# Performance work log

Hardware: AMD Instinct MI355X
Metric: run time of the kernel (lower is better)

The kernel has to match this reference:

```python
import jax, jax.numpy as jnp
import numpy as np

B, T, H, OUT = 128, 1024, 256, 2


def setup_inputs() -> dict:
    key = jax.random.key(0)
    ks = jax.random.split(key, 16)
    s_in = 1.0 / np.sqrt(1 + H)
    s_2h = 1.0 / np.sqrt(2 * H)
    s_o = 1.0 / np.sqrt(H)
    return {
        "x": jax.random.normal(ks[0], (B, T, 2), dtype=jnp.float32),
        "h_0": jax.random.normal(ks[1], (1, B, H), dtype=jnp.float32) * 0.1,
        "Wa": jax.random.normal(ks[2], (1 + H, H), dtype=jnp.float32) * s_in,
        "ba": jnp.zeros((H,), dtype=jnp.float32),
        "Wp1": jax.random.normal(ks[3], (1 + H, H), dtype=jnp.float32) * s_in,
        "bp1": jnp.zeros((H,), dtype=jnp.float32),
        "Wp2": jax.random.normal(ks[4], (1 + H, H), dtype=jnp.float32) * s_in,
        "bp2": jnp.zeros((H,), dtype=jnp.float32),
        "Wz": jax.random.normal(ks[5], (2 * H, H), dtype=jnp.float32) * s_2h,
        "bz": jnp.zeros((H,), dtype=jnp.float32),
        "Wh": jax.random.normal(ks[6], (2 * H, H), dtype=jnp.float32) * s_2h,
        "bh": jnp.zeros((H,), dtype=jnp.float32),
        "Wo": jax.random.normal(ks[7], (H, OUT), dtype=jnp.float32) * s_o,
        "bo": jnp.zeros((OUT,), dtype=jnp.float32),
    }


def _pgjanet_scan(x, h0, Wa, ba, Wp1, bp1, Wp2, bp2, Wz, bz, Wh, bh):
    # x: [B, T, 2], h0: [B, H]
    xt_all = jnp.swapaxes(x, 0, 1)  # [T, B, 2]

    def step(h, xt):
        amp = xt[:, 0:1]                       # [B, 1]
        ph = xt[:, 1:2]                        # [B, 1]
        a = jnp.tanh(jnp.concatenate([amp, h], axis=-1) @ Wa + ba)
        p1 = jnp.tanh(jnp.concatenate([jnp.cos(ph), h], axis=-1) @ Wp1 + bp1)
        p2 = jnp.tanh(jnp.concatenate([jnp.sin(ph), h], axis=-1) @ Wp2 + bp2)
        u = a * p1 * p2 * (1 - a) * (1 - p1) * (1 - p2)
        newin = jnp.concatenate([u, h], axis=-1)  # [B, 2H]
        z = jax.nn.sigmoid(newin @ Wz + bz)
        h_cand = jnp.tanh(newin @ Wh + bh)
        h_new = z * h + (1 - z) * h_cand
        return h_new, h_new

    h_n, hs = jax.lax.scan(step, h0, xt_all)
    return jnp.swapaxes(hs, 0, 1), h_n  # [B, T, H], [B, H]


def reference(x, h_0, Wa, ba, Wp1, bp1, Wp2, bp2, Wz, bz, Wh, bh, Wo, bo):
    hs, h_n = _pgjanet_scan(x, h_0[0], Wa, ba, Wp1, bp1, Wp2, bp2, Wz, bz, Wh, bh)
    out = hs @ Wo + bo  # [B, T, OUT]
    return (out, h_n)
```

## Files before the change

### kernel.cpp

```cpp
#include <hip/hip_runtime.h>
#include <math.h>


#define B_   128
#define T_   1024
#define H_   256
#define GB   16
#define GC   16
#define MB   8
#define NS   16
#define NTHR 512
#define HPAD 264

typedef float    f32x4 __attribute__((ext_vector_type(4)));
typedef unsigned u32x4 __attribute__((ext_vector_type(4)));

__device__ __forceinline__ void sys_st_x4(unsigned* p, u32x4 v) {
  asm volatile("global_store_dwordx4 %0, %1, off sc0 sc1" :: "v"(p), "v"(v) : "memory");
}
__device__ __forceinline__ void sys_ld2_x4(const unsigned* p0, const unsigned* p1,
                                           u32x4& a, u32x4& b) {
  asm volatile("global_load_dwordx4 %0, %2, off sc0 sc1\n\t"
               "global_load_dwordx4 %1, %3, off sc0 sc1\n\t"
               "s_waitcnt vmcnt(0)"
               : "=&v"(a), "=&v"(b) : "v"(p0), "v"(p1) : "memory");
}

__launch_bounds__(NTHR, 1)
__global__ void pgjanet_persist(
    const float* __restrict__ x,   const float* __restrict__ h0,
    const float* __restrict__ Wa,  const float* __restrict__ ba,
    const float* __restrict__ Wp1, const float* __restrict__ bp1,
    const float* __restrict__ Wp2, const float* __restrict__ bp2,
    const float* __restrict__ Wz,  const float* __restrict__ bz,
    const float* __restrict__ Wh,  const float* __restrict__ bh,
    const float* __restrict__ Wo,  const float* __restrict__ bo,
    float* __restrict__ out,
    unsigned* __restrict__ u_ex,
    unsigned* __restrict__ h_ex)
{
  __shared__ __align__(16) float w1t[3 * NS * 256];
  __shared__ __align__(16) float w2t[2 * NS * 512];
  __shared__ __align__(16) float h_lds[MB * HPAD];
  __shared__ __align__(16) float u_lds[MB * HPAD];
  __shared__ __align__(16) float wo_s[H_ * 2];
  __shared__ __align__(16) float xin[2 * MB * 4];

  const int wg   = blockIdx.x;
  const int g    = wg >> 4;
  const int gc   = wg & (GC - 1);
  const int tid  = threadIdx.x;
  const int lane = tid & 63;
  const int wave = tid >> 6;
  const int mb   = lane >> 3;
  const int ks   = lane & 7;
  const int b0   = g * MB;
  const int n0   = gc * NS + wave * 2;

  for (int i = tid; i < 3 * NS * 256; i += NTHR) {
    int c = i >> 8, k = i & 255;
    int mat = c >> 4, n = c & 15;
    const float* W = (mat == 0) ? Wa : (mat == 1 ? Wp1 : Wp2);
    w1t[i] = W[(1 + k) * H_ + gc * NS + n];
  }
  for (int i = tid; i < 2 * NS * 512; i += NTHR) {
    int c = i >> 9, k = i & 511;
    int mat = c >> 4, n = c & 15;
    const float* W = (mat == 0) ? Wz : Wh;
    w2t[i] = W[k * H_ + gc * NS + n];
  }
  for (int i = tid; i < H_ * 2; i += NTHR) wo_s[i] = Wo[i];

  float w1r0_[6], b1_[6];
#pragma unroll
  for (int m = 0; m < 3; ++m) {
    const float* W  = (m == 0) ? Wa : (m == 1 ? Wp1 : Wp2);
    const float* bb = (m == 0) ? ba : (m == 1 ? bp1 : bp2);
#pragma unroll
    for (int cc = 0; cc < 2; ++cc) {
      w1r0_[m * 2 + cc] = W[n0 + cc];
      b1_[m * 2 + cc]   = bb[n0 + cc];
    }
  }
  float bz_[2] = { bz[n0], bz[n0 + 1] };
  float bh_[2] = { bh[n0], bh[n0 + 1] };
  const float bo0 = bo[0], bo1 = bo[1];

  {
    int flat = tid * 4;
    int mbb = flat >> 8, kk = flat & 255;
    *(f32x4*)(h_lds + mbb * HPAD + kk) = *(const f32x4*)(h0 + (b0 + mbb) * H_ + kk);
  }
  if (tid < MB) {
    float2 xt = *(const float2*)(x + ((b0 + tid) * T_) * 2);
    f32x4 xi; xi[0] = xt.x; xi[1] = cosf(xt.y); xi[2] = sinf(xt.y); xi[3] = 0.f;
    *(f32x4*)(xin + tid * 4) = xi;
  }
  __syncthreads();

  unsigned* u_exg = u_ex + g * 4096;
  unsigned* h_exg = h_ex + g * 4096;
  unsigned* u_my  = u_exg + ((gc * 8 + wave) * 8) * 4;
  unsigned* h_my  = h_exg + ((gc * 8 + wave) * 8) * 4;

  for (int t = 0; t < T_; ++t) {
    const unsigned seq = (unsigned)(t + 1);

    f32x4 hv[8];
#pragma unroll
    for (int kt = 0; kt < 8; ++kt)
      hv[kt] = *(const f32x4*)(h_lds + mb * HPAD + kt * 32 + ks * 4);

    float acc[6] = {0.f, 0.f, 0.f, 0.f, 0.f, 0.f};
#pragma unroll
    for (int kt = 0; kt < 8; ++kt) {
      f32x4 h4 = hv[kt];
#pragma unroll
      for (int m = 0; m < 3; ++m)
#pragma unroll
        for (int cc = 0; cc < 2; ++cc) {
          f32x4 w4 = *(const f32x4*)(w1t + (m * NS + wave * 2 + cc) * 256 + kt * 32 + ks * 4);
          float s = acc[m * 2 + cc];
          s = fmaf(h4[0], w4[0], s); s = fmaf(h4[1], w4[1], s);
          s = fmaf(h4[2], w4[2], s); s = fmaf(h4[3], w4[3], s);
          acc[m * 2 + cc] = s;
        }
    }
#pragma unroll
    for (int i = 0; i < 6; ++i) {
      float v = acc[i];
      v += __shfl_xor(v, 1);
      v += __shfl_xor(v, 2);
      v += __shfl_xor(v, 4);
      acc[i] = v;
    }
    if (ks == 0) {
      f32x4 xi = *(const f32x4*)(xin + ((t & 1) * MB + mb) * 4);
      float uu[2];
#pragma unroll
      for (int cc = 0; cc < 2; ++cc) {
        float a  = tanhf(acc[0 + cc] + xi[0] * w1r0_[0 + cc] + b1_[0 + cc]);
        float p1 = tanhf(acc[2 + cc] + xi[1] * w1r0_[2 + cc] + b1_[2 + cc]);
        float p2 = tanhf(acc[4 + cc] + xi[2] * w1r0_[4 + cc] + b1_[4 + cc]);
        uu[cc] = a * p1 * p2 * (1.f - a) * (1.f - p1) * (1.f - p2);
      }
      u32x4 ch;
      ch.x = __float_as_uint(uu[0]); ch.y = __float_as_uint(uu[1]);
      ch.z = seq; ch.w = 0u;
      sys_st_x4(u_my + mb * 4, ch);
    }

    if (t + 1 < T_ && tid < MB) {
      float2 xt = *(const float2*)(x + ((b0 + tid) * T_ + (t + 1)) * 2);
      f32x4 xi; xi[0] = xt.x; xi[1] = cosf(xt.y); xi[2] = sinf(xt.y); xi[3] = 0.f;
      *(f32x4*)(xin + (((t + 1) & 1) * MB + tid) * 4) = xi;
    }
    if (t > 0 && ((t - 1) & 15) == gc) {
      f32x4 h4  = *(const f32x4*)(h_lds + wave * HPAD + lane * 4);
      f32x4 wo0 = *(const f32x4*)(wo_s + lane * 8);
      f32x4 wo1 = *(const f32x4*)(wo_s + lane * 8 + 4);
      float v0 = h4[0] * wo0[0] + h4[1] * wo0[2] + h4[2] * wo1[0] + h4[3] * wo1[2];
      float v1 = h4[0] * wo0[1] + h4[1] * wo0[3] + h4[2] * wo1[1] + h4[3] * wo1[3];
      v0 += __shfl_xor(v0, 1);  v1 += __shfl_xor(v1, 1);
      v0 += __shfl_xor(v0, 2);  v1 += __shfl_xor(v1, 2);
      v0 += __shfl_xor(v0, 4);  v1 += __shfl_xor(v1, 4);
      v0 += __shfl_xor(v0, 8);  v1 += __shfl_xor(v1, 8);
      v0 += __shfl_xor(v0, 16); v1 += __shfl_xor(v1, 16);
      v0 += __shfl_xor(v0, 32); v1 += __shfl_xor(v1, 32);
      if (lane == 0) {
        float2 o; o.x = v0 + bo0; o.y = v1 + bo1;
        *(float2*)(out + ((b0 + wave) * T_ + (t - 1)) * 2) = o;
      }
    }
    float acc2[4] = {0.f, 0.f, 0.f, 0.f};
#pragma unroll
    for (int kt = 0; kt < 8; ++kt) {
      f32x4 h4 = hv[kt];
#pragma unroll
      for (int m = 0; m < 2; ++m)
#pragma unroll
        for (int cc = 0; cc < 2; ++cc) {
          f32x4 w4 = *(const f32x4*)(w2t + (m * NS + wave * 2 + cc) * 512 + 256 + kt * 32 + ks * 4);
          float s = acc2[m * 2 + cc];
          s = fmaf(h4[0], w4[0], s); s = fmaf(h4[1], w4[1], s);
          s = fmaf(h4[2], w4[2], s); s = fmaf(h4[3], w4[3], s);
          acc2[m * 2 + cc] = s;
        }
    }

    {
      u32x4 A, B;
      const unsigned* p0 = u_exg + tid * 4;
      const unsigned* p1 = u_exg + (tid + 512) * 4;
      for (;;) {
        sys_ld2_x4(p0, p1, A, B);
        if (A.z == seq && B.z == seq) break;
        __builtin_amdgcn_s_sleep(1);
      }
      int c = tid;
      float2 d0; d0.x = __uint_as_float(A.x); d0.y = __uint_as_float(A.y);
      *(float2*)(u_lds + (c & 7) * HPAD + (c >> 6) * 16 + ((c >> 3) & 7) * 2) = d0;
      c = tid + 512;
      float2 d1; d1.x = __uint_as_float(B.x); d1.y = __uint_as_float(B.y);
      *(float2*)(u_lds + (c & 7) * HPAD + (c >> 6) * 16 + ((c >> 3) & 7) * 2) = d1;
    }
    __syncthreads();

#pragma unroll
    for (int kt = 0; kt < 8; ++kt) {
      f32x4 u4 = *(const f32x4*)(u_lds + mb * HPAD + kt * 32 + ks * 4);
#pragma unroll
      for (int m = 0; m < 2; ++m)
#pragma unroll
        for (int cc = 0; cc < 2; ++cc) {
          f32x4 w4 = *(const f32x4*)(w2t + (m * NS + wave * 2 + cc) * 512 + kt * 32 + ks * 4);
          float s = acc2[m * 2 + cc];
          s = fmaf(u4[0], w4[0], s); s = fmaf(u4[1], w4[1], s);
          s = fmaf(u4[2], w4[2], s); s = fmaf(u4[3], w4[3], s);
          acc2[m * 2 + cc] = s;
        }
    }
#pragma unroll
    for (int i = 0; i < 4; ++i) {
      float v = acc2[i];
      v += __shfl_xor(v, 1);
      v += __shfl_xor(v, 2);
      v += __shfl_xor(v, 4);
      acc2[i] = v;
    }
    if (ks == 0) {
      float z0  = 1.f / (1.f + expf(-(acc2[0] + bz_[0])));
      float z1  = 1.f / (1.f + expf(-(acc2[1] + bz_[1])));
      float hc0 = tanhf(acc2[2] + bh_[0]);
      float hc1 = tanhf(acc2[3] + bh_[1]);
      float2 hp = *(const float2*)(h_lds + mb * HPAD + n0);
      float hn0 = z0 * hp.x + (1.f - z0) * hc0;
      float hn1 = z1 * hp.y + (1.f - z1) * hc1;
      u32x4 ch;
      ch.x = __float_as_uint(hn0); ch.y = __float_as_uint(hn1);
      ch.z = seq; ch.w = 0u;
      sys_st_x4(h_my + mb * 4, ch);
      if (t == T_ - 1) {
        float2 o; o.x = hn0; o.y = hn1;
        *(float2*)(out + B_ * T_ * 2 + (b0 + mb) * H_ + n0) = o;
      }
    }
    __syncthreads();

    {
      u32x4 A, B;
      const unsigned* p0 = h_exg + tid * 4;
      const unsigned* p1 = h_exg + (tid + 512) * 4;
      for (;;) {
        sys_ld2_x4(p0, p1, A, B);
        if (A.z == seq && B.z == seq) break;
        __builtin_amdgcn_s_sleep(1);
      }
      int c = tid;
      float2 d0; d0.x = __uint_as_float(A.x); d0.y = __uint_as_float(A.y);
      *(float2*)(h_lds + (c & 7) * HPAD + (c >> 6) * 16 + ((c >> 3) & 7) * 2) = d0;
      c = tid + 512;
      float2 d1; d1.x = __uint_as_float(B.x); d1.y = __uint_as_float(B.y);
      *(float2*)(h_lds + (c & 7) * HPAD + (c >> 6) * 16 + ((c >> 3) & 7) * 2) = d1;
    }
    __syncthreads();
  }

  if (gc == ((T_ - 1) & 15)) {
    f32x4 h4  = *(const f32x4*)(h_lds + wave * HPAD + lane * 4);
    f32x4 wo0 = *(const f32x4*)(wo_s + lane * 8);
    f32x4 wo1 = *(const f32x4*)(wo_s + lane * 8 + 4);
    float v0 = h4[0] * wo0[0] + h4[1] * wo0[2] + h4[2] * wo1[0] + h4[3] * wo1[2];
    float v1 = h4[0] * wo0[1] + h4[1] * wo0[3] + h4[2] * wo1[1] + h4[3] * wo1[3];
    v0 += __shfl_xor(v0, 1);  v1 += __shfl_xor(v1, 1);
    v0 += __shfl_xor(v0, 2);  v1 += __shfl_xor(v1, 2);
    v0 += __shfl_xor(v0, 4);  v1 += __shfl_xor(v1, 4);
    v0 += __shfl_xor(v0, 8);  v1 += __shfl_xor(v1, 8);
    v0 += __shfl_xor(v0, 16); v1 += __shfl_xor(v1, 16);
    v0 += __shfl_xor(v0, 32); v1 += __shfl_xor(v1, 32);
    if (lane == 0) {
      float2 o; o.x = v0 + bo0; o.y = v1 + bo1;
      *(float2*)(out + ((b0 + wave) * T_ + (T_ - 1)) * 2) = o;
    }
  }
}

extern "C" void kernel_launch(void* const* d_in, const int* in_sizes, int n_in,
                              void* d_out, int out_size, void* d_ws, size_t ws_size,
                              hipStream_t stream) {
  (void)in_sizes; (void)n_in; (void)out_size; (void)ws_size;
  const float* x   = (const float*)d_in[0];
  const float* h0  = (const float*)d_in[1];
  const float* Wa  = (const float*)d_in[2];
  const float* ba  = (const float*)d_in[3];
  const float* Wp1 = (const float*)d_in[4];
  const float* bp1 = (const float*)d_in[5];
  const float* Wp2 = (const float*)d_in[6];
  const float* bp2 = (const float*)d_in[7];
  const float* Wz  = (const float*)d_in[8];
  const float* bz  = (const float*)d_in[9];
  const float* Wh  = (const float*)d_in[10];
  const float* bh  = (const float*)d_in[11];
  const float* Wo  = (const float*)d_in[12];
  const float* bo  = (const float*)d_in[13];

  float* out = (float*)d_out;
  char*  ws  = (char*)d_ws;
  unsigned* u_ex = (unsigned*)ws;
  unsigned* h_ex = (unsigned*)(ws + 262144);

  hipMemsetAsync(ws, 0, 524288, stream);

  pgjanet_persist<<<dim3(GB * GC), dim3(NTHR), 0, stream>>>(
      x, h0, Wa, ba, Wp1, bp1, Wp2, bp2, Wz, bz, Wh, bh, Wo, bo,
      out, u_ex, h_ex);
}
```

Baseline: 5.698 ms.

## Split batch into two halves per wave, widen K-split, use fast tanh/sigmoid

Each wave now handles two groups of four batch rows with a 16-way K split instead of eight rows with an 8-way split. Each weight vector loaded from LDS is reused for both halves in the h-part of the second GEMV. The exchange layout is reordered so each thread polls two adjacent 16-byte slots from one base pointer, and the first half's u is published earlier. tanhf/expf are replaced by clamped __expf with a hardware reciprocal, which is cheaper but slightly less accurate.

```diff
diff --git a/kernel.cpp b/kernel.cpp
--- a/kernel.cpp
+++ b/kernel.cpp
@@ -18,12 +18,21 @@
 __device__ __forceinline__ void sys_st_x4(unsigned* p, u32x4 v) {
   asm volatile("global_store_dwordx4 %0, %1, off sc0 sc1" :: "v"(p), "v"(v) : "memory");
 }
-__device__ __forceinline__ void sys_ld2_x4(const unsigned* p0, const unsigned* p1,
-                                           u32x4& a, u32x4& b) {
+__device__ __forceinline__ void sys_ld_pair(const unsigned* p, u32x4& a, u32x4& b) {
   asm volatile("global_load_dwordx4 %0, %2, off sc0 sc1\n\t"
-               "global_load_dwordx4 %1, %3, off sc0 sc1\n\t"
+               "global_load_dwordx4 %1, %2, off offset:16 sc0 sc1\n\t"
                "s_waitcnt vmcnt(0)"
-               : "=&v"(a), "=&v"(b) : "v"(p0), "v"(p1) : "memory");
+               : "=&v"(a), "=&v"(b) : "v"(p) : "memory");
+}
+
+__device__ __forceinline__ float ftanh(float x) {
+  x = fminf(fmaxf(x, -15.f), 15.f);
+  float e = __expf(-2.f * x);
+  return (1.f - e) * __builtin_amdgcn_rcpf(1.f + e);
+}
+__device__ __forceinline__ float fsigm(float x) {
+  x = fminf(fmaxf(x, -30.f), 30.f);
+  return __builtin_amdgcn_rcpf(1.f + __expf(-x));
 }
 
 __launch_bounds__(NTHR, 1)
@@ -52,8 +61,8 @@
   const int tid  = threadIdx.x;
   const int lane = tid & 63;
   const int wave = tid >> 6;
-  const int mb   = lane >> 3;
-  const int ks   = lane & 7;
+  const int mbl  = lane >> 4;
+  const int ks   = lane & 15;
   const int b0   = g * MB;
   const int n0   = gc * NS + wave * 2;
 
@@ -87,8 +96,7 @@
   const float bo0 = bo[0], bo1 = bo[1];
 
   {
-    int flat = tid * 4;
-    int mbb = flat >> 8, kk = flat & 255;
+    int mbb = tid >> 6, kk = (tid & 63) * 4;
     *(f32x4*)(h_lds + mbb * HPAD + kk) = *(const f32x4*)(h0 + (b0 + mbb) * H_ + kk);
   }
   if (tid < MB) {
@@ -100,54 +108,101 @@
 
   unsigned* u_exg = u_ex + g * 4096;
   unsigned* h_exg = h_ex + g * 4096;
-  unsigned* u_my  = u_exg + ((gc * 8 + wave) * 8) * 4;
-  unsigned* h_my  = h_exg + ((gc * 8 + wave) * 8) * 4;
+  unsigned* u_my = u_exg + (((gc * 8 + wave) * 4 + mbl) * 2) * 4;
+  unsigned* h_my = h_exg + (((gc * 8 + wave) * 4 + mbl) * 2) * 4;
+  const unsigned* pu = u_exg + tid * 8;
+  const unsigned* ph = h_exg + tid * 8;
+  const int ccol = (tid >> 5) * 16 + ((tid >> 2) & 7) * 2;
+  const int cmb  = tid & 3;
 
   for (int t = 0; t < T_; ++t) {
     const unsigned seq = (unsigned)(t + 1);
 
-    f32x4 hv[8];
-#pragma unroll
-    for (int kt = 0; kt < 8; ++kt)
-      hv[kt] = *(const f32x4*)(h_lds + mb * HPAD + kt * 32 + ks * 4);
-
-    float acc[6] = {0.f, 0.f, 0.f, 0.f, 0.f, 0.f};
-#pragma unroll
-    for (int kt = 0; kt < 8; ++kt) {
-      f32x4 h4 = hv[kt];
-#pragma unroll
-      for (int m = 0; m < 3; ++m)
-#pragma unroll
-        for (int cc = 0; cc < 2; ++cc) {
-          f32x4 w4 = *(const f32x4*)(w1t + (m * NS + wave * 2 + cc) * 256 + kt * 32 + ks * 4);
-          float s = acc[m * 2 + cc];
-          s = fmaf(h4[0], w4[0], s); s = fmaf(h4[1], w4[1], s);
-          s = fmaf(h4[2], w4[2], s); s = fmaf(h4[3], w4[3], s);
-          acc[m * 2 + cc] = s;
-        }
-    }
-#pragma unroll
-    for (int i = 0; i < 6; ++i) {
-      float v = acc[i];
-      v += __shfl_xor(v, 1);
-      v += __shfl_xor(v, 2);
-      v += __shfl_xor(v, 4);
-      acc[i] = v;
-    }
-    if (ks == 0) {
-      f32x4 xi = *(const f32x4*)(xin + ((t & 1) * MB + mb) * 4);
-      float uu[2];
-#pragma unroll
-      for (int cc = 0; cc < 2; ++cc) {
-        float a  = tanhf(acc[0 + cc] + xi[0] * w1r0_[0 + cc] + b1_[0 + cc]);
-        float p1 = tanhf(acc[2 + cc] + xi[1] * w1r0_[2 + cc] + b1_[2 + cc]);
-        float p2 = tanhf(acc[4 + cc] + xi[2] * w1r0_[4 + cc] + b1_[4 + cc]);
-        uu[cc] = a * p1 * p2 * (1.f - a) * (1.f - p1) * (1.f - p2);
-      }
-      u32x4 ch;
-      ch.x = __float_as_uint(uu[0]); ch.y = __float_as_uint(uu[1]);
-      ch.z = seq; ch.w = 0u;
-      sys_st_x4(u_my + mb * 4, ch);
+    f32x4 hvA[4], hvB[4];
+    float acc2A[4] = {0.f, 0.f, 0.f, 0.f};
+    float acc2B[4] = {0.f, 0.f, 0.f, 0.f};
+
+#pragma unroll
+    for (int kt = 0; kt < 4; ++kt)
+      hvA[kt] = *(const f32x4*)(h_lds + mbl * HPAD + kt * 64 + ks * 4);
+    {
+      float acc[6] = {0.f, 0.f, 0.f, 0.f, 0.f, 0.f};
+#pragma unroll
+      for (int kt = 0; kt < 4; ++kt) {
+        f32x4 h4 = hvA[kt];
+#pragma unroll
+        for (int m = 0; m < 3; ++m)
+#pragma unroll
+          for (int cc = 0; cc < 2; ++cc) {
+            f32x4 w4 = *(const f32x4*)(w1t + (m * NS + wave * 2 + cc) * 256 + kt * 64 + ks * 4);
+            float s = acc[m * 2 + cc];
+            s = fmaf(h4[0], w4[0], s); s = fmaf(h4[1], w4[1], s);
+            s = fmaf(h4[2], w4[2], s); s = fmaf(h4[3], w4[3], s);
+            acc[m * 2 + cc] = s;
+          }
+      }
+#pragma unroll
+      for (int i = 0; i < 6; ++i) {
+        float v = acc[i];
+        v += __shfl_xor(v, 1); v += __shfl_xor(v, 2);
+        v += __shfl_xor(v, 4); v += __shfl_xor(v, 8);
+        acc[i] = v;
+      }
+      if (ks == 0) {
+        f32x4 xi = *(const f32x4*)(xin + ((t & 1) * MB + mbl) * 4);
+        float a0  = ftanh(acc[0] + xi[0] * w1r0_[0] + b1_[0]);
+        float a1  = ftanh(acc[1] + xi[0] * w1r0_[1] + b1_[1]);
+        float p10 = ftanh(acc[2] + xi[1] * w1r0_[2] + b1_[2]);
+        float p11 = ftanh(acc[3] + xi[1] * w1r0_[3] + b1_[3]);
+        float p20 = ftanh(acc[4] + xi[2] * w1r0_[4] + b1_[4]);
+        float p21 = ftanh(acc[5] + xi[2] * w1r0_[5] + b1_[5]);
+        u32x4 ch;
+        ch.x = __float_as_uint(a0 * p10 * p20 * (1.f - a0) * (1.f - p10) * (1.f - p20));
+        ch.y = __float_as_uint(a1 * p11 * p21 * (1.f - a1) * (1.f - p11) * (1.f - p21));
+        ch.z = seq; ch.w = 0u;
+        sys_st_x4(u_my, ch);
+      }
+    }
+#pragma unroll
+    for (int kt = 0; kt < 4; ++kt)
+      hvB[kt] = *(const f32x4*)(h_lds + (4 + mbl) * HPAD + kt * 64 + ks * 4);
+    {
+      float acc[6] = {0.f, 0.f, 0.f, 0.f, 0.f, 0.f};
+#pragma unroll
+      for (int kt = 0; kt < 4; ++kt) {
+        f32x4 h4 = hvB[kt];
+#pragma unroll
+        for (int m = 0; m < 3; ++m)
+#pragma unroll
+          for (int cc = 0; cc < 2; ++cc) {
+            f32x4 w4 = *(const f32x4*)(w1t + (m * NS + wave * 2 + cc) * 256 + kt * 64 + ks * 4);
+            float s = acc[m * 2 + cc];
+            s = fmaf(h4[0], w4[0], s); s = fmaf(h4[1], w4[1], s);
+            s = fmaf(h4[2], w4[2], s); s = fmaf(h4[3], w4[3], s);
+            acc[m * 2 + cc] = s;
+          }
+      }
+#pragma unroll
+      for (int i = 0; i < 6; ++i) {
+        float v = acc[i];
+        v += __shfl_xor(v, 1); v += __shfl_xor(v, 2);
+        v += __shfl_xor(v, 4); v += __shfl_xor(v, 8);
+        acc[i] = v;
+      }
+      if (ks == 0) {
+        f32x4 xi = *(const f32x4*)(xin + ((t & 1) * MB + 4 + mbl) * 4);
+        float a0  = ftanh(acc[0] + xi[0] * w1r0_[0] + b1_[0]);
+        float a1  = ftanh(acc[1] + xi[0] * w1r0_[1] + b1_[1]);
+        float p10 = ftanh(acc[2] + xi[1] * w1r0_[2] + b1_[2]);
+        float p11 = ftanh(acc[3] + xi[1] * w1r0_[3] + b1_[3]);
+        float p20 = ftanh(acc[4] + xi[2] * w1r0_[4] + b1_[4]);
+        float p21 = ftanh(acc[5] + xi[2] * w1r0_[5] + b1_[5]);
+        u32x4 ch;
+        ch.x = __float_as_uint(a0 * p10 * p20 * (1.f - a0) * (1.f - p10) * (1.f - p20));
+        ch.y = __float_as_uint(a1 * p11 * p21 * (1.f - a1) * (1.f - p11) * (1.f - p21));
+        ch.z = seq; ch.w = 0u;
+        sys_st_x4(u_my + 4, ch);
+      }
     }
 
     if (t + 1 < T_ && tid < MB) {
@@ -172,96 +227,126 @@
         *(float2*)(out + ((b0 + wave) * T_ + (t - 1)) * 2) = o;
       }
     }
-    float acc2[4] = {0.f, 0.f, 0.f, 0.f};
-#pragma unroll
-    for (int kt = 0; kt < 8; ++kt) {
-      f32x4 h4 = hv[kt];
+#pragma unroll
+    for (int kt = 0; kt < 4; ++kt) {
+      f32x4 hA = hvA[kt], hB = hvB[kt];
 #pragma unroll
       for (int m = 0; m < 2; ++m)
 #pragma unroll
         for (int cc = 0; cc < 2; ++cc) {
-          f32x4 w4 = *(const f32x4*)(w2t + (m * NS + wave * 2 + cc) * 512 + 256 + kt * 32 + ks * 4);
-          float s = acc2[m * 2 + cc];
-          s = fmaf(h4[0], w4[0], s); s = fmaf(h4[1], w4[1], s);
-          s = fmaf(h4[2], w4[2], s); s = fmaf(h4[3], w4[3], s);
-          acc2[m * 2 + cc] = s;
+          f32x4 w4 = *(const f32x4*)(w2t + (m * NS + wave * 2 + cc) * 512 + 256 + kt * 64 + ks * 4);
+          float sa = acc2A[m * 2 + cc], sb = acc2B[m * 2 + cc];
+          sa = fmaf(hA[0], w4[0], sa); sa = fmaf(hA[1], w4[1], sa);
+          sa = fmaf(hA[2], w4[2], sa); sa = fmaf(hA[3], w4[3], sa);
+          sb = fmaf(hB[0], w4[0], sb); sb = fmaf(hB[1], w4[1], sb);
+          sb = fmaf(hB[2], w4[2], sb); sb = fmaf(hB[3], w4[3], sb);
+          acc2A[m * 2 + cc] = sa; acc2B[m * 2 + cc] = sb;
         }
     }
 
     {
-      u32x4 A, B;
-      const unsigned* p0 = u_exg + tid * 4;
-      const unsigned* p1 = u_exg + (tid + 512) * 4;
+      u32x4 A, Bc;
       for (;;) {
-        sys_ld2_x4(p0, p1, A, B);
-        if (A.z == seq && B.z == seq) break;
+        sys_ld_pair(pu, A, Bc);
+        if (A.z == seq && Bc.z == seq) break;
         __builtin_amdgcn_s_sleep(1);
       }
-      int c = tid;
-      float2 d0; d0.x = __uint_as_float(A.x); d0.y = __uint_as_float(A.y);
-      *(float2*)(u_lds + (c & 7) * HPAD + (c >> 6) * 16 + ((c >> 3) & 7) * 2) = d0;
-      c = tid + 512;
-      float2 d1; d1.x = __uint_as_float(B.x); d1.y = __uint_as_float(B.y);
-      *(float2*)(u_lds + (c & 7) * HPAD + (c >> 6) * 16 + ((c >> 3) & 7) * 2) = d1;
+      float2 d0; d0.x = __uint_as_float(A.x);  d0.y = __uint_as_float(A.y);
+      float2 d1; d1.x = __uint_as_float(Bc.x); d1.y = __uint_as_float(Bc.y);
+      *(float2*)(u_lds + cmb * HPAD + ccol)       = d0;
+      *(float2*)(u_lds + (cmb + 4) * HPAD + ccol) = d1;
     }
     __syncthreads();
 
 #pragma unroll
-    for (int kt = 0; kt < 8; ++kt) {
-      f32x4 u4 = *(const f32x4*)(u_lds + mb * HPAD + kt * 32 + ks * 4);
+    for (int kt = 0; kt < 4; ++kt) {
+      f32x4 u4 = *(const f32x4*)(u_lds + mbl * HPAD + kt * 64 + ks * 4);
 #pragma unroll
       for (int m = 0; m < 2; ++m)
 #pragma unroll
         for (int cc = 0; cc < 2; ++cc) {
-          f32x4 w4 = *(const f32x4*)(w2t + (m * NS + wave * 2 + cc) * 512 + kt * 32 + ks * 4);
-          float s = acc2[m * 2 + cc];
+          f32x4 w4 = *(const f32x4*)(w2t + (m * NS + wave * 2 + cc) * 512 + kt * 64 + ks * 4);
+          float s = acc2A[m * 2 + cc];
           s = fmaf(u4[0], w4[0], s); s = fmaf(u4[1], w4[1], s);
           s = fmaf(u4[2], w4[2], s); s = fmaf(u4[3], w4[3], s);
-          acc2[m * 2 + cc] = s;
+          acc2A[m * 2 + cc] = s;
         }
     }
 #pragma unroll
     for (int i = 0; i < 4; ++i) {
-      float v = acc2[i];
-      v += __shfl_xor(v, 1);
-      v += __shfl_xor(v, 2);
-      v += __shfl_xor(v, 4);
-      acc2[i] = v;
+      float v = acc2A[i];
+      v += __shfl_xor(v, 1); v += __shfl_xor(v, 2);
+      v += __shfl_xor(v, 4); v += __shfl_xor(v, 8);
+      acc2A[i] = v;
     }
     if (ks == 0) {
-      float z0  = 1.f / (1.f + expf(-(acc2[0] + bz_[0])));
-      float z1  = 1.f / (1.f + expf(-(acc2[1] + bz_[1])));
-      float hc0 = tanhf(acc2[2] + bh_[0]);
-      float hc1 = tanhf(acc2[3] + bh_[1]);
-      float2 hp = *(const float2*)(h_lds + mb * HPAD + n0);
+      float z0  = fsigm(acc2A[0] + bz_[0]);
+      float z1  = fsigm(acc2A[1] + bz_[1]);
+      float hc0 = ftanh(acc2A[2] + bh_[0]);
+      float hc1 = ftanh(acc2A[3] + bh_[1]);
+      float2 hp = *(const float2*)(h_lds + mbl * HPAD + n0);
       float hn0 = z0 * hp.x + (1.f - z0) * hc0;
       float hn1 = z1 * hp.y + (1.f - z1) * hc1;
       u32x4 ch;
       ch.x = __float_as_uint(hn0); ch.y = __float_as_uint(hn1);
       ch.z = seq; ch.w = 0u;
-      sys_st_x4(h_my + mb * 4, ch);
+      sys_st_x4(h_my, ch);
       if (t == T_ - 1) {
         float2 o; o.x = hn0; o.y = hn1;
-        *(float2*)(out + B_ * T_ * 2 + (b0 + mb) * H_ + n0) = o;
+        *(float2*)(out + B_ * T_ * 2 + (b0 + mbl) * H_ + n0) = o;
+      }
+    }
+#pragma unroll
+    for (int kt = 0; kt < 4; ++kt) {
+      f32x4 u4 = *(const f32x4*)(u_lds + (4 + mbl) * HPAD + kt * 64 + ks * 4);
+#pragma unroll
+      for (int m = 0; m < 2; ++m)
+#pragma unroll
+        for (int cc = 0; cc < 2; ++cc) {
+          f32x4 w4 = *(const f32x4*)(w2t + (m * NS + wave * 2 + cc) * 512 + kt * 64 + ks * 4);
+          float s = acc2B[m * 2 + cc];
+          s = fmaf(u4[0], w4[0], s); s = fmaf(u4[1], w4[1], s);
+          s = fmaf(u4[2], w4[2], s); s = fmaf(u4[3], w4[3], s);
+          acc2B[m * 2 + cc] = s;
+        }
+    }
+#pragma unroll
+    for (int i = 0; i < 4; ++i) {
+      float v = acc2B[i];
+      v += __shfl_xor(v, 1); v += __shfl_xor(v, 2);
+      v += __shfl_xor(v, 4); v += __shfl_xor(v, 8);
+      acc2B[i] = v;
+    }
+    if (ks == 0) {
+      float z0  = fsigm(acc2B[0] + bz_[0]);
+      float z1  = fsigm(acc2B[1] + bz_[1]);
+      float hc0 = ftanh(acc2B[2] + bh_[0]);
+      float hc1 = ftanh(acc2B[3] + bh_[1]);
+      float2 hp = *(const float2*)(h_lds + (4 + mbl) * HPAD + n0);
+      float hn0 = z0 * hp.x + (1.f - z0) * hc0;
+      float hn1 = z1 * hp.y + (1.f - z1) * hc1;
+      u32x4 ch;
+      ch.x = __float_as_uint(hn0); ch.y = __float_as_uint(hn1);
+      ch.z = seq; ch.w = 0u;
+      sys_st_x4(h_my + 4, ch);
+      if (t == T_ - 1) {
+        float2 o; o.x = hn0; o.y = hn1;
+        *(float2*)(out + B_ * T_ * 2 + (b0 + 4 + mbl) * H_ + n0) = o;
       }
     }
     __syncthreads();
 
     {
-      u32x4 A, B;
-      const unsigned* p0 = h_exg + tid * 4;
-      const unsigned* p1 = h_exg + (tid + 512) * 4;
+      u32x4 A, Bc;
       for (;;) {
-        sys_ld2_x4(p0, p1, A, B);
-        if (A.z == seq && B.z == seq) break;
+        sys_ld_pair(ph, A, Bc);
+        if (A.z == seq && Bc.z == seq) break;
         __builtin_amdgcn_s_sleep(1);
       }
-      int c = tid;
-      float2 d0; d0.x = __uint_as_float(A.x); d0.y = __uint_as_float(A.y);
-      *(float2*)(h_lds + (c & 7) * HPAD + (c >> 6) * 16 + ((c >> 3) & 7) * 2) = d0;
-      c = tid + 512;
-      float2 d1; d1.x = __uint_as_float(B.x); d1.y = __uint_as_float(B.y);
-      *(float2*)(h_lds + (c & 7) * HPAD + (c >> 6) * 16 + ((c >> 3) & 7) * 2) = d1;
+      float2 d0; d0.x = __uint_as_float(A.x);  d0.y = __uint_as_float(A.y);
+      float2 d1; d1.x = __uint_as_float(Bc.x); d1.y = __uint_as_float(Bc.y);
+      *(float2*)(h_lds + cmb * HPAD + ccol)       = d0;
+      *(float2*)(h_lds + (cmb + 4) * HPAD + ccol) = d1;
     }
     __syncthreads();
   }
```

Result: slower. 6.873 ms (+20.6%).

## Split hidden columns across 32 smaller workgroups and use fast tanh/sigmoid

Applied to the files above, without the earlier changes.

Doubles the number of workgroups per batch group (each now owns 8 hidden columns with 256 threads), so per-step matmul work per workgroup halves and two workgroups can share a CU. The exchange polling is reorganised so each thread loads four contiguous 16-byte chunks with one base pointer. Library tanhf/expf are replaced by clamped exp plus hardware reciprocal approximations. The trade-off is more workgroups taking part in each per-step global flag exchange, which may raise synchronisation latency, and slightly lower accuracy in the activations.

```diff
diff --git a/kernel.cpp b/kernel.cpp
--- a/kernel.cpp
+++ b/kernel.cpp
@@ -6,10 +6,10 @@
 #define T_   1024
 #define H_   256
 #define GB   16
-#define GC   16
+#define GC   32
 #define MB   8
-#define NS   16
-#define NTHR 512
+#define NS   8
+#define NTHR 256
 #define HPAD 264
 
 typedef float    f32x4 __attribute__((ext_vector_type(4)));
@@ -18,15 +18,27 @@
 __device__ __forceinline__ void sys_st_x4(unsigned* p, u32x4 v) {
   asm volatile("global_store_dwordx4 %0, %1, off sc0 sc1" :: "v"(p), "v"(v) : "memory");
 }
-__device__ __forceinline__ void sys_ld2_x4(const unsigned* p0, const unsigned* p1,
-                                           u32x4& a, u32x4& b) {
-  asm volatile("global_load_dwordx4 %0, %2, off sc0 sc1\n\t"
-               "global_load_dwordx4 %1, %3, off sc0 sc1\n\t"
+__device__ __forceinline__ void sys_ld_quad(const unsigned* p, u32x4& a, u32x4& b,
+                                            u32x4& c, u32x4& d) {
+  asm volatile("global_load_dwordx4 %0, %4, off sc0 sc1\n\t"
+               "global_load_dwordx4 %1, %4, off offset:16 sc0 sc1\n\t"
+               "global_load_dwordx4 %2, %4, off offset:32 sc0 sc1\n\t"
+               "global_load_dwordx4 %3, %4, off offset:48 sc0 sc1\n\t"
                "s_waitcnt vmcnt(0)"
-               : "=&v"(a), "=&v"(b) : "v"(p0), "v"(p1) : "memory");
-}
-
-__launch_bounds__(NTHR, 1)
+               : "=&v"(a), "=&v"(b), "=&v"(c), "=&v"(d) : "v"(p) : "memory");
+}
+
+__device__ __forceinline__ float ftanh(float x) {
+  x = fminf(fmaxf(x, -15.f), 15.f);
+  float e = __expf(-2.f * x);
+  return (1.f - e) * __builtin_amdgcn_rcpf(1.f + e);
+}
+__device__ __forceinline__ float fsigm(float x) {
+  x = fminf(fmaxf(x, -30.f), 30.f);
+  return __builtin_amdgcn_rcpf(1.f + __expf(-x));
+}
+
+__launch_bounds__(NTHR, 2)
 __global__ void pgjanet_persist(
     const float* __restrict__ x,   const float* __restrict__ h0,
     const float* __restrict__ Wa,  const float* __restrict__ ba,
@@ -47,7 +59,7 @@
   __shared__ __align__(16) float xin[2 * MB * 4];
 
   const int wg   = blockIdx.x;
-  const int g    = wg >> 4;
+  const int g    = wg >> 5;
   const int gc   = wg & (GC - 1);
   const int tid  = threadIdx.x;
   const int lane = tid & 63;
@@ -59,13 +71,13 @@
 
   for (int i = tid; i < 3 * NS * 256; i += NTHR) {
     int c = i >> 8, k = i & 255;
-    int mat = c >> 4, n = c & 15;
+    int mat = c >> 3, n = c & 7;
     const float* W = (mat == 0) ? Wa : (mat == 1 ? Wp1 : Wp2);
     w1t[i] = W[(1 + k) * H_ + gc * NS + n];
   }
   for (int i = tid; i < 2 * NS * 512; i += NTHR) {
     int c = i >> 9, k = i & 511;
-    int mat = c >> 4, n = c & 15;
+    int mat = c >> 3, n = c & 7;
     const float* W = (mat == 0) ? Wz : Wh;
     w2t[i] = W[k * H_ + gc * NS + n];
   }
@@ -87,9 +99,9 @@
   const float bo0 = bo[0], bo1 = bo[1];
 
   {
-    int flat = tid * 4;
-    int mbb = flat >> 8, kk = flat & 255;
-    *(f32x4*)(h_lds + mbb * HPAD + kk) = *(const f32x4*)(h0 + (b0 + mbb) * H_ + kk);
+    int mbb = tid >> 5, kk = (tid & 31) * 8;
+    *(f32x4*)(h_lds + mbb * HPAD + kk)     = *(const f32x4*)(h0 + (b0 + mbb) * H_ + kk);
+    *(f32x4*)(h_lds + mbb * HPAD + kk + 4) = *(const f32x4*)(h0 + (b0 + mbb) * H_ + kk + 4);
   }
   if (tid < MB) {
     float2 xt = *(const float2*)(x + ((b0 + tid) * T_) * 2);
@@ -100,8 +112,12 @@
 
   unsigned* u_exg = u_ex + g * 4096;
   unsigned* h_exg = h_ex + g * 4096;
-  unsigned* u_my  = u_exg + ((gc * 8 + wave) * 8) * 4;
-  unsigned* h_my  = h_exg + ((gc * 8 + wave) * 8) * 4;
+  unsigned* u_my  = u_exg + ((gc * 4 + wave) * 8) * 4;
+  unsigned* h_my  = h_exg + ((gc * 4 + wave) * 8) * 4;
+  const unsigned* pu = u_exg + tid * 16;
+  const unsigned* ph = h_exg + tid * 16;
+  const int crow0 = (tid & 1) * 4;
+  const int ccol  = (tid >> 1) * 2;
 
   for (int t = 0; t < T_; ++t) {
     const unsigned seq = (unsigned)(t + 1);
@@ -129,23 +145,20 @@
 #pragma unroll
     for (int i = 0; i < 6; ++i) {
       float v = acc[i];
-      v += __shfl_xor(v, 1);
-      v += __shfl_xor(v, 2);
-      v += __shfl_xor(v, 4);
+      v += __shfl_xor(v, 1); v += __shfl_xor(v, 2); v += __shfl_xor(v, 4);
       acc[i] = v;
     }
     if (ks == 0) {
       f32x4 xi = *(const f32x4*)(xin + ((t & 1) * MB + mb) * 4);
-      float uu[2];
-#pragma unroll
-      for (int cc = 0; cc < 2; ++cc) {
-        float a  = tanhf(acc[0 + cc] + xi[0] * w1r0_[0 + cc] + b1_[0 + cc]);
-        float p1 = tanhf(acc[2 + cc] + xi[1] * w1r0_[2 + cc] + b1_[2 + cc]);
-        float p2 = tanhf(acc[4 + cc] + xi[2] * w1r0_[4 + cc] + b1_[4 + cc]);
-        uu[cc] = a * p1 * p2 * (1.f - a) * (1.f - p1) * (1.f - p2);
-      }
+      float a0  = ftanh(acc[0] + xi[0] * w1r0_[0] + b1_[0]);
+      float a1  = ftanh(acc[1] + xi[0] * w1r0_[1] + b1_[1]);
+      float p10 = ftanh(acc[2] + xi[1] * w1r0_[2] + b1_[2]);
+      float p11 = ftanh(acc[3] + xi[1] * w1r0_[3] + b1_[3]);
+      float p20 = ftanh(acc[4] + xi[2] * w1r0_[4] + b1_[4]);
+      float p21 = ftanh(acc[5] + xi[2] * w1r0_[5] + b1_[5]);
       u32x4 ch;
-      ch.x = __float_as_uint(uu[0]); ch.y = __float_as_uint(uu[1]);
+      ch.x = __float_as_uint(a0 * p10 * p20 * (1.f - a0) * (1.f - p10) * (1.f - p20));
+      ch.y = __float_as_uint(a1 * p11 * p21 * (1.f - a1) * (1.f - p11) * (1.f - p21));
       ch.z = seq; ch.w = 0u;
       sys_st_x4(u_my + mb * 4, ch);
     }
@@ -155,21 +168,28 @@
       f32x4 xi; xi[0] = xt.x; xi[1] = cosf(xt.y); xi[2] = sinf(xt.y); xi[3] = 0.f;
       *(f32x4*)(xin + (((t + 1) & 1) * MB + tid) * 4) = xi;
     }
-    if (t > 0 && ((t - 1) & 15) == gc) {
-      f32x4 h4  = *(const f32x4*)(h_lds + wave * HPAD + lane * 4);
-      f32x4 wo0 = *(const f32x4*)(wo_s + lane * 8);
-      f32x4 wo1 = *(const f32x4*)(wo_s + lane * 8 + 4);
-      float v0 = h4[0] * wo0[0] + h4[1] * wo0[2] + h4[2] * wo1[0] + h4[3] * wo1[2];
-      float v1 = h4[0] * wo0[1] + h4[1] * wo0[3] + h4[2] * wo1[1] + h4[3] * wo1[3];
+    if (t > 0 && ((t - 1) & (GC - 1)) == gc) {
+      int bb = wave * 2 + (lane >> 5);
+      int kk = (lane & 31) * 8;
+      const float* hr = h_lds + bb * HPAD + kk;
+      f32x4 h4a = *(const f32x4*)(hr);
+      f32x4 h4b = *(const f32x4*)(hr + 4);
+      float v0 = 0.f, v1 = 0.f;
+#pragma unroll
+      for (int j = 0; j < 4; ++j) {
+        v0 = fmaf(h4a[j], wo_s[(kk + j) * 2 + 0], v0);
+        v1 = fmaf(h4a[j], wo_s[(kk + j) * 2 + 1], v1);
+        v0 = fmaf(h4b[j], wo_s[(kk + 4 + j) * 2 + 0], v0);
+        v1 = fmaf(h4b[j], wo_s[(kk + 4 + j) * 2 + 1], v1);
+      }
       v0 += __shfl_xor(v0, 1);  v1 += __shfl_xor(v1, 1);
       v0 += __shfl_xor(v0, 2);  v1 += __shfl_xor(v1, 2);
       v0 += __shfl_xor(v0, 4);  v1 += __shfl_xor(v1, 4);
       v0 += __shfl_xor(v0, 8);  v1 += __shfl_xor(v1, 8);
       v0 += __shfl_xor(v0, 16); v1 += __shfl_xor(v1, 16);
-      v0 += __shfl_xor(v0, 32); v1 += __shfl_xor(v1, 32);
-      if (lane == 0) {
+      if ((lane & 31) == 0) {
         float2 o; o.x = v0 + bo0; o.y = v1 + bo1;
-        *(float2*)(out + ((b0 + wave) * T_ + (t - 1)) * 2) = o;
+        *(float2*)(out + ((b0 + bb) * T_ + (t - 1)) * 2) = o;
       }
     }
     float acc2[4] = {0.f, 0.f, 0.f, 0.f};
@@ -189,20 +209,21 @@
     }
 
     {
-      u32x4 A, B;
-      const unsigned* p0 = u_exg + tid * 4;
-      const unsigned* p1 = u_exg + (tid + 512) * 4;
+      u32x4 A, Bq, Cq, Dq;
       for (;;) {
-        sys_ld2_x4(p0, p1, A, B);
-        if (A.z == seq && B.z == seq) break;
+        sys_ld_quad(pu, A, Bq, Cq, Dq);
+        if (A.z == seq && Bq.z == seq && Cq.z == seq && Dq.z == seq) break;
         __builtin_amdgcn_s_sleep(1);
       }
-      int c = tid;
-      float2 d0; d0.x = __uint_as_float(A.x); d0.y = __uint_as_float(A.y);
-      *(float2*)(u_lds + (c & 7) * HPAD + (c >> 6) * 16 + ((c >> 3) & 7) * 2) = d0;
-      c = tid + 512;
-      float2 d1; d1.x = __uint_as_float(B.x); d1.y = __uint_as_float(B.y);
-      *(float2*)(u_lds + (c & 7) * HPAD + (c >> 6) * 16 + ((c >> 3) & 7) * 2) = d1;
+      float2 d;
+      d.x = __uint_as_float(A.x);  d.y = __uint_as_float(A.y);
+      *(float2*)(u_lds + (crow0 + 0) * HPAD + ccol) = d;
+      d.x = __uint_as_float(Bq.x); d.y = __uint_as_float(Bq.y);
+      *(float2*)(u_lds + (crow0 + 1) * HPAD + ccol) = d;
+      d.x = __uint_as_float(Cq.x); d.y = __uint_as_float(Cq.y);
+      *(float2*)(u_lds + (crow0 + 2) * HPAD + ccol) = d;
+      d.x = __uint_as_float(Dq.x); d.y = __uint_as_float(Dq.y);
+      *(float2*)(u_lds + (crow0 + 3) * HPAD + ccol) = d;
     }
     __syncthreads();
 
@@ -223,16 +244,14 @@
 #pragma unroll
     for (int i = 0; i < 4; ++i) {
       float v = acc2[i];
-      v += __shfl_xor(v, 1);
-      v += __shfl_xor(v, 2);
-      v += __shfl_xor(v, 4);
+      v += __shfl_xor(v, 1); v += __shfl_xor(v, 2); v += __shfl_xor(v, 4);
       acc2[i] = v;
     }
     if (ks == 0) {
-      float z0  = 1.f / (1.f + expf(-(acc2[0] + bz_[0])));
-      float z1  = 1.f / (1.f + expf(-(acc2[1] + bz_[1])));
-      float hc0 = tanhf(acc2[2] + bh_[0]);
-      float hc1 = tanhf(acc2[3] + bh_[1]);
+      float z0  = fsigm(acc2[0] + bz_[0]);
+      float z1  = fsigm(acc2[1] + bz_[1]);
+      float hc0 = ftanh(acc2[2] + bh_[0]);
+      float hc1 = ftanh(acc2[3] + bh_[1]);
       float2 hp = *(const float2*)(h_lds + mb * HPAD + n0);
       float hn0 = z0 * hp.x + (1.f - z0) * hc0;
       float hn1 = z1 * hp.y + (1.f - z1) * hc1;
@@ -248,39 +267,47 @@
     __syncthreads();
 
     {
-      u32x4 A, B;
-      const unsigned* p0 = h_exg + tid * 4;
-      const unsigned* p1 = h_exg + (tid + 512) * 4;
+      u32x4 A, Bq, Cq, Dq;
       for (;;) {
-        sys_ld2_x4(p0, p1, A, B);
-        if (A.z == seq && B.z == seq) break;
+        sys_ld_quad(ph, A, Bq, Cq, Dq);
+        if (A.z == seq && Bq.z == seq && Cq.z == seq && Dq.z == seq) break;
         __builtin_amdgcn_s_sleep(1);
       }
-      int c = tid;
-      float2 d0; d0.x = __uint_as_float(A.x); d0.y = __uint_as_float(A.y);
-      *(float2*)(h_lds + (c & 7) * HPAD + (c >> 6) * 16 + ((c >> 3) & 7) * 2) = d0;
-      c = tid + 512;
-      float2 d1; d1.x = __uint_as_float(B.x); d1.y = __uint_as_float(B.y);
-      *(float2*)(h_lds + (c & 7) * HPAD + (c >> 6) * 16 + ((c >> 3) & 7) * 2) = d1;
+      float2 d;
+      d.x = __uint_as_float(A.x);  d.y = __uint_as_float(A.y);
+      *(float2*)(h_lds + (crow0 + 0) * HPAD + ccol) = d;
+      d.x = __uint_as_float(Bq.x); d.y = __uint_as_float(Bq.y);
+      *(float2*)(h_lds + (crow0 + 1) * HPAD + ccol) = d;
+      d.x = __uint_as_float(Cq.x); d.y = __uint_as_float(Cq.y);
+      *(float2*)(h_lds + (crow0 + 2) * HPAD + ccol) = d;
+      d.x = __uint_as_float(Dq.x); d.y = __uint_as_float(Dq.y);
+      *(float2*)(h_lds + (crow0 + 3) * HPAD + ccol) = d;
     }
     __syncthreads();
   }
 
-  if (gc == ((T_ - 1) & 15)) {
-    f32x4 h4  = *(const f32x4*)(h_lds + wave * HPAD + lane * 4);
-    f32x4 wo0 = *(const f32x4*)(wo_s + lane * 8);
-    f32x4 wo1 = *(const f32x4*)(wo_s + lane * 8 + 4);
-    float v0 = h4[0] * wo0[0] + h4[1] * wo0[2] + h4[2] * wo1[0] + h4[3] * wo1[2];
-    float v1 = h4[0] * wo0[1] + h4[1] * wo0[3] + h4[2] * wo1[1] + h4[3] * wo1[3];
+  if (gc == ((T_ - 1) & (GC - 1))) {
+    int bb = wave * 2 + (lane >> 5);
+    int kk = (lane & 31) * 8;
+    const float* hr = h_lds + bb * HPAD + kk;
+    f32x4 h4a = *(const f32x4*)(hr);
+    f32x4 h4b = *(const f32x4*)(hr + 4);
+    float v0 = 0.f, v1 = 0.f;
+#pragma unroll
+    for (int j = 0; j < 4; ++j) {
+      v0 = fmaf(h4a[j], wo_s[(kk + j) * 2 + 0], v0);
+      v1 = fmaf(h4a[j], wo_s[(kk + j) * 2 + 1], v1);
+      v0 = fmaf(h4b[j], wo_s[(kk + 4 + j) * 2 + 0], v0);
+      v1 = fmaf(h4b[j], wo_s[(kk + 4 + j) * 2 + 1], v1);
+    }
     v0 += __shfl_xor(v0, 1);  v1 += __shfl_xor(v1, 1);
     v0 += __shfl_xor(v0, 2);  v1 += __shfl_xor(v1, 2);
     v0 += __shfl_xor(v0, 4);  v1 += __shfl_xor(v1, 4);
     v0 += __shfl_xor(v0, 8);  v1 += __shfl_xor(v1, 8);
     v0 += __shfl_xor(v0, 16); v1 += __shfl_xor(v1, 16);
-    v0 += __shfl_xor(v0, 32); v1 += __shfl_xor(v1, 32);
-    if (lane == 0) {
+    if ((lane & 31) == 0) {
       float2 o; o.x = v0 + bo0; o.y = v1 + bo1;
-      *(float2*)(out + ((b0 + wave) * T_ + (T_ - 1)) * 2) = o;
+      *(float2*)(out + ((b0 + bb) * T_ + (T_ - 1)) * 2) = o;
     }
   }
 }
```

After: 9.446 ms. 65.8% more time.
